# Kernel tuning notes

Hardware: AMD Instinct MI355X
Metric: run time of the kernel (lower is better)

## Reference

```python
import jax, jax.numpy as jnp
import numpy as np

K = 8            # hard-attention top-k neighbors per node
NEG_SLOPE = 0.2  # leaky relu slope


def setup_inputs() -> dict:
    key = jax.random.key(0)
    k1, k2, k3, k4, k5, k6 = jax.random.split(key, 6)
    N, D, F = 50000, 64, 256
    H, O = 8, 32
    feat = jax.random.normal(k1, (N, F), dtype=jnp.float32)
    neighbors = jax.random.randint(k2, (N, D), 0, N)  # src node ids per dst
    # learned params (xavier-normal-ish scale)
    p = jax.random.normal(k3, (1, F), dtype=jnp.float32) * float(np.sqrt(2.0 / (1 + F)))
    W = jax.random.normal(k4, (F, H * O), dtype=jnp.float32) * float(np.sqrt(2.0 / (F + H * O)))
    attn_l = jax.random.normal(k5, (1, H, O), dtype=jnp.float32) * float(np.sqrt(2.0 / (H * O + 1)))
    attn_r = jax.random.normal(k6, (1, H, O), dtype=jnp.float32) * float(np.sqrt(2.0 / (H * O + 1)))
    return {"feat": feat, "neighbors": neighbors, "p": p, "W": W,
            "attn_l": attn_l, "attn_r": attn_r}


def reference(feat, neighbors, p, W, attn_l, attn_r):
    N, F = feat.shape
    H, O = attn_l.shape[1], attn_l.shape[2]
    # node projection score y = |p . x| / ||p||
    y = jnp.abs(feat @ p[0]) / jnp.linalg.norm(p)          # [N]
    # hard top-k neighbor selection by source score (select_topk on 'y')
    ys = y[neighbors]                                       # [N, D]
    _, idx = jax.lax.top_k(ys, K)                           # [N, K]
    src = jnp.take_along_axis(neighbors, idx, axis=1)       # [N, K] source ids
    # gating + projection
    gate = jax.nn.sigmoid(y) * 2.0                          # [N]
    ft = ((gate[:, None] * feat) @ W).reshape(N, H, O)      # [N, H, O]
    el = jnp.sum(ft * attn_l, axis=-1)                      # [N, H]
    er = jnp.sum(ft * attn_r, axis=-1)                      # [N, H]
    # edge scores: u_add_v, leaky_relu, edge_softmax over each dst's K edges
    e = el[src] + er[:, None, :]                            # [N, K, H]
    e = jnp.where(e > 0, e, NEG_SLOPE * e)
    a = jax.nn.softmax(e, axis=1)                           # [N, K, H]
    # u_mul_e + sum aggregation
    rst = jnp.einsum('nkh,nkho->nho', a, ft[src])           # [N, H, O]
    return jax.nn.elu(rst)
```

## Files before the change

kernel.cpp:

```cpp
#include <hip/hip_runtime.h>
#include <math.h>

#define NEG_SLOPE 0.2f

typedef _Float16 half8 __attribute__((ext_vector_type(8)));
typedef float floatx4 __attribute__((ext_vector_type(4)));

__device__ __forceinline__ float dot4f(float4 a, float4 b) {
    return a.x * b.x + a.y * b.y + a.z * b.z + a.w * b.w;
}

static __device__ __forceinline__ unsigned short f2h(float x) {
    _Float16 h = (_Float16)x;
    return __builtin_bit_cast(unsigned short, h);
}
static __device__ __forceinline__ float h2f(unsigned short u) {
    _Float16 h = __builtin_bit_cast(_Float16, u);
    return (float)h;
}

__global__ void k_prepw(const float* __restrict__ W, unsigned short* __restrict__ Wtp) {
    const int c = blockIdx.x;
    const int k = threadIdx.x;
    float v = W[(size_t)k * 256 + c];
    Wtp[(size_t)(c >> 4) * 4096 + (k >> 3) * 128 + (c & 15) * 8 + (k & 7)] = f2h(v);
}

__global__ __launch_bounds__(256) void k_fused(const float4* __restrict__ feat4,
                                               const float4* __restrict__ p4,
                                               const unsigned short* __restrict__ Wtp,
                                               float* __restrict__ y,
                                               unsigned short* __restrict__ fth,
                                               int N) {
    __shared__ unsigned short As[16][264];
    const int lane = threadIdx.x & 63;
    const int w = threadIdx.x >> 6;
    const int l16 = lane & 15, quad = lane >> 4;
    const int nb = blockIdx.x * 16;

    const float4 p = p4[lane];
    float pp = dot4f(p, p);
#pragma unroll
    for (int off = 32; off; off >>= 1) pp += __shfl_xor(pp, off, 64);
    const float rnorm = 1.0f / sqrtf(pp);

#pragma unroll
    for (int j = 0; j < 4; ++j) {
        const int m = w * 4 + j;
        int n = nb + m;
        const bool valid = n < N;
        if (!valid) n = N - 1;
        float4 f = feat4[(size_t)n * 64 + lane];
        float dp = dot4f(f, p);
#pragma unroll
        for (int off = 32; off; off >>= 1) dp += __shfl_xor(dp, off, 64);
        float yv = fabsf(dp) * rnorm;
        if (lane == 0 && valid) y[n] = yv;
        float g = 2.0f / (1.0f + expf(-yv));
        ushort4 u;
        u.x = f2h(g * f.x);
        u.y = f2h(g * f.y);
        u.z = f2h(g * f.z);
        u.w = f2h(g * f.w);
        *(ushort4*)&As[m][lane * 4] = u;
    }
    __syncthreads();

    floatx4 acc[4];
#pragma unroll
    for (int ct = 0; ct < 4; ++ct) acc[ct] = (floatx4){0.f, 0.f, 0.f, 0.f};

    const unsigned short* bbase = Wtp + (size_t)(w * 4) * 4096 + quad * 128 + l16 * 8;

    for (int ks = 0; ks < 256; ks += 32) {
        half8 a = *(const half8*)&As[l16][ks + quad * 8];
        const unsigned short* bk = bbase + (ks >> 3) * 128;
        half8 b0 = *(const half8*)(bk);
        half8 b1 = *(const half8*)(bk + 4096);
        half8 b2 = *(const half8*)(bk + 8192);
        half8 b3 = *(const half8*)(bk + 12288);
        acc[0] = __builtin_amdgcn_mfma_f32_16x16x32_f16(a, b0, acc[0], 0, 0, 0);
        acc[1] = __builtin_amdgcn_mfma_f32_16x16x32_f16(a, b1, acc[1], 0, 0, 0);
        acc[2] = __builtin_amdgcn_mfma_f32_16x16x32_f16(a, b2, acc[2], 0, 0, 0);
        acc[3] = __builtin_amdgcn_mfma_f32_16x16x32_f16(a, b3, acc[3], 0, 0, 0);
    }

#pragma unroll
    for (int ct = 0; ct < 4; ++ct)
#pragma unroll
        for (int i = 0; i < 4; ++i) {
            int row = nb + quad * 4 + i;
            if (row < N)
                fth[(size_t)row * 256 + w * 64 + ct * 16 + l16] = f2h(acc[ct][i]);
        }
}

__global__ __launch_bounds__(256) void k_aggr(const int* __restrict__ nbr,
                                              const float* __restrict__ y,
                                              const uint2* __restrict__ fth2,
                                              const float4* __restrict__ al4,
                                              const float4* __restrict__ ar4,
                                              float4* __restrict__ out4,
                                              int N) {
    const int lane = threadIdx.x & 63;
    const int n = blockIdx.x * 4 + (threadIdx.x >> 6);
    if (n >= N) return;

    const int s = nbr[(size_t)n * 64 + lane];
    const unsigned int key = __float_as_uint(y[s]);

    unsigned int t = 0u;
#pragma unroll
    for (int b = 31; b >= 0; --b) {
        unsigned int cand = t | (1u << b);
        unsigned long long m = __ballot(key >= cand);
        if (__popcll(m) >= 8) t = cand;
    }
    const unsigned long long gtmask = __ballot(key > t);
    const int ngt = __popcll(gtmask);
    const unsigned long long eqmask = __ballot(key == t);
    const unsigned long long below = (1ull << lane) - 1ull;
    const int eqrank = __popcll(eqmask & below);
    const bool in8 = (key > t) | ((key == t) & (eqrank < 8 - ngt));
    unsigned long long selmask = __ballot(in8);

    int srck[8];
#pragma unroll
    for (int k = 0; k < 8; ++k) {
        int l = __ffsll((long long)selmask) - 1;
        srck[k] = __shfl(s, l, 64);
        selmask &= selmask - 1ull;
    }

    float4 ftn, ftk[8];
    {
        uint2 v = fth2[(size_t)n * 64 + lane];
        ftn.x = h2f((unsigned short)(v.x & 0xffff));
        ftn.y = h2f((unsigned short)(v.x >> 16));
        ftn.z = h2f((unsigned short)(v.y & 0xffff));
        ftn.w = h2f((unsigned short)(v.y >> 16));
    }
#pragma unroll
    for (int k = 0; k < 8; ++k) {
        uint2 v = fth2[(size_t)srck[k] * 64 + lane];
        ftk[k].x = h2f((unsigned short)(v.x & 0xffff));
        ftk[k].y = h2f((unsigned short)(v.x >> 16));
        ftk[k].z = h2f((unsigned short)(v.y & 0xffff));
        ftk[k].w = h2f((unsigned short)(v.y >> 16));
    }

    const float4 al = al4[lane];
    const float4 ar = ar4[lane];

    float er = dot4f(ftn, ar);
#pragma unroll
    for (int off = 1; off < 8; off <<= 1) er += __shfl_xor(er, off, 64);

    float e[8];
#pragma unroll
    for (int k = 0; k < 8; ++k) {
        float el = dot4f(ftk[k], al);
#pragma unroll
        for (int off = 1; off < 8; off <<= 1) el += __shfl_xor(el, off, 64);
        float ev = el + er;
        e[k] = ev > 0.f ? ev : NEG_SLOPE * ev;
    }

    float m = e[0];
#pragma unroll
    for (int k = 1; k < 8; ++k) m = fmaxf(m, e[k]);
    float sum = 0.f;
#pragma unroll
    for (int k = 0; k < 8; ++k) {
        e[k] = expf(e[k] - m);
        sum += e[k];
    }
    const float inv = 1.0f / sum;

    float4 acc = make_float4(0.f, 0.f, 0.f, 0.f);
#pragma unroll
    for (int k = 0; k < 8; ++k) {
        float a = e[k] * inv;
        acc.x += a * ftk[k].x;
        acc.y += a * ftk[k].y;
        acc.z += a * ftk[k].z;
        acc.w += a * ftk[k].w;
    }
    acc.x = acc.x > 0.f ? acc.x : expf(acc.x) - 1.f;
    acc.y = acc.y > 0.f ? acc.y : expf(acc.y) - 1.f;
    acc.z = acc.z > 0.f ? acc.z : expf(acc.z) - 1.f;
    acc.w = acc.w > 0.f ? acc.w : expf(acc.w) - 1.f;
    out4[(size_t)n * 64 + lane] = acc;
}

extern "C" void kernel_launch(void* const* d_in, const int* in_sizes, int n_in,
                              void* d_out, int out_size, void* d_ws, size_t ws_size,
                              hipStream_t stream) {
    const float* feat = (const float*)d_in[0];
    const int* nbr    = (const int*)d_in[1];
    const float* p    = (const float*)d_in[2];
    const float* W    = (const float*)d_in[3];
    const float* al   = (const float*)d_in[4];
    const float* ar   = (const float*)d_in[5];
    float* out = (float*)d_out;

    const int N = in_sizes[0] / 256;

    float* y = (float*)d_ws;
    unsigned short* Wtp = (unsigned short*)(y + N);
    unsigned short* fth = Wtp + 256 * 256;

    k_prepw<<<256, 256, 0, stream>>>(W, Wtp);
    k_fused<<<(N + 15) / 16, 256, 0, stream>>>((const float4*)feat, (const float4*)p,
                                               Wtp, y, fth, N);
    k_aggr<<<(N + 3) / 4, 256, 0, stream>>>(nbr, y, (const uint2*)fth,
                                            (const float4*)al, (const float4*)ar,
                                            (float4*)out, N);
}
```

Before: 176.6 us.

## Precompute el/er in GEMM epilogue, double GEMM row tile, use fast exp

The projection kernel now handles 32 rows per block (two MFMA M-tiles reusing each loaded W fragment). It stages the fp16 result in shared memory and computes the per-head attention terms el and er there, writing them to workspace. The aggregation kernel then reads el/er instead of recomputing dot products and shuffle reductions for each of the 8 neighbors, and it no longer loads the destination row's features. Other changes: __expf replaces expf, and the top-k bit search skips the sign bit. These add workspace traffic and shared-memory use and slightly reduce exp accuracy.

```diff
diff --git a/kernel.cpp b/kernel.cpp
--- a/kernel.cpp
+++ b/kernel.cpp
@@ -29,14 +29,18 @@
 __global__ __launch_bounds__(256) void k_fused(const float4* __restrict__ feat4,
                                                const float4* __restrict__ p4,
                                                const unsigned short* __restrict__ Wtp,
+                                               const float4* __restrict__ al4,
+                                               const float4* __restrict__ ar4,
                                                float* __restrict__ y,
                                                unsigned short* __restrict__ fth,
+                                               float* __restrict__ el,
+                                               float* __restrict__ er,
                                                int N) {
-    __shared__ unsigned short As[16][264];
+    __shared__ unsigned short As[32][264];
     const int lane = threadIdx.x & 63;
     const int w = threadIdx.x >> 6;
     const int l16 = lane & 15, quad = lane >> 4;
-    const int nb = blockIdx.x * 16;
+    const int nb = blockIdx.x * 32;
 
     const float4 p = p4[lane];
     float pp = dot4f(p, p);
@@ -45,8 +49,8 @@
     const float rnorm = 1.0f / sqrtf(pp);
 
 #pragma unroll
-    for (int j = 0; j < 4; ++j) {
-        const int m = w * 4 + j;
+    for (int j = 0; j < 8; ++j) {
+        const int m = w * 8 + j;
         int n = nb + m;
         const bool valid = n < N;
         if (!valid) n = N - 1;
@@ -56,7 +60,7 @@
         for (int off = 32; off; off >>= 1) dp += __shfl_xor(dp, off, 64);
         float yv = fabsf(dp) * rnorm;
         if (lane == 0 && valid) y[n] = yv;
-        float g = 2.0f / (1.0f + expf(-yv));
+        float g = 2.0f / (1.0f + __expf(-yv));
         ushort4 u;
         u.x = f2h(g * f.x);
         u.y = f2h(g * f.y);
@@ -66,52 +70,83 @@
     }
     __syncthreads();
 
-    floatx4 acc[4];
-#pragma unroll
-    for (int ct = 0; ct < 4; ++ct) acc[ct] = (floatx4){0.f, 0.f, 0.f, 0.f};
+    floatx4 acc[2][4];
+#pragma unroll
+    for (int mt = 0; mt < 2; ++mt)
+#pragma unroll
+        for (int ct = 0; ct < 4; ++ct) acc[mt][ct] = (floatx4){0.f, 0.f, 0.f, 0.f};
 
     const unsigned short* bbase = Wtp + (size_t)(w * 4) * 4096 + quad * 128 + l16 * 8;
 
     for (int ks = 0; ks < 256; ks += 32) {
-        half8 a = *(const half8*)&As[l16][ks + quad * 8];
+        half8 a0 = *(const half8*)&As[l16][ks + quad * 8];
+        half8 a1 = *(const half8*)&As[16 + l16][ks + quad * 8];
         const unsigned short* bk = bbase + (ks >> 3) * 128;
         half8 b0 = *(const half8*)(bk);
         half8 b1 = *(const half8*)(bk + 4096);
         half8 b2 = *(const half8*)(bk + 8192);
         half8 b3 = *(const half8*)(bk + 12288);
-        acc[0] = __builtin_amdgcn_mfma_f32_16x16x32_f16(a, b0, acc[0], 0, 0, 0);
-        acc[1] = __builtin_amdgcn_mfma_f32_16x16x32_f16(a, b1, acc[1], 0, 0, 0);
-        acc[2] = __builtin_amdgcn_mfma_f32_16x16x32_f16(a, b2, acc[2], 0, 0, 0);
-        acc[3] = __builtin_amdgcn_mfma_f32_16x16x32_f16(a, b3, acc[3], 0, 0, 0);
-    }
-
-#pragma unroll
-    for (int ct = 0; ct < 4; ++ct)
-#pragma unroll
-        for (int i = 0; i < 4; ++i) {
-            int row = nb + quad * 4 + i;
-            if (row < N)
-                fth[(size_t)row * 256 + w * 64 + ct * 16 + l16] = f2h(acc[ct][i]);
+        acc[0][0] = __builtin_amdgcn_mfma_f32_16x16x32_f16(a0, b0, acc[0][0], 0, 0, 0);
+        acc[0][1] = __builtin_amdgcn_mfma_f32_16x16x32_f16(a0, b1, acc[0][1], 0, 0, 0);
+        acc[0][2] = __builtin_amdgcn_mfma_f32_16x16x32_f16(a0, b2, acc[0][2], 0, 0, 0);
+        acc[0][3] = __builtin_amdgcn_mfma_f32_16x16x32_f16(a0, b3, acc[0][3], 0, 0, 0);
+        acc[1][0] = __builtin_amdgcn_mfma_f32_16x16x32_f16(a1, b0, acc[1][0], 0, 0, 0);
+        acc[1][1] = __builtin_amdgcn_mfma_f32_16x16x32_f16(a1, b1, acc[1][1], 0, 0, 0);
+        acc[1][2] = __builtin_amdgcn_mfma_f32_16x16x32_f16(a1, b2, acc[1][2], 0, 0, 0);
+        acc[1][3] = __builtin_amdgcn_mfma_f32_16x16x32_f16(a1, b3, acc[1][3], 0, 0, 0);
+    }
+
+    __syncthreads();
+#pragma unroll
+    for (int mt = 0; mt < 2; ++mt)
+#pragma unroll
+        for (int ct = 0; ct < 4; ++ct)
+#pragma unroll
+            for (int i = 0; i < 4; ++i) {
+                int row = mt * 16 + quad * 4 + i;
+                int col = w * 64 + ct * 16 + l16;
+                unsigned short h = f2h(acc[mt][ct][i]);
+                As[row][col] = h;
+                int grow = nb + row;
+                if (grow < N) fth[(size_t)grow * 256 + col] = h;
+            }
+    __syncthreads();
+
+#pragma unroll
+    for (int t2 = 0; t2 < 2; ++t2) {
+        const int m = threadIdx.x & 31;
+        const int h = (threadIdx.x >> 5) & 7;
+        const float4* att = t2 ? ar4 : al4;
+        float d = 0.f;
+#pragma unroll
+        for (int o4 = 0; o4 < 8; ++o4) {
+            ushort4 u = *(const ushort4*)&As[m][h * 32 + o4 * 4];
+            float4 a = att[h * 8 + o4];
+            d += h2f(u.x) * a.x + h2f(u.y) * a.y + h2f(u.z) * a.z + h2f(u.w) * a.w;
         }
+        int n = nb + m;
+        if (n < N) (t2 ? er : el)[(size_t)n * 8 + h] = d;
+    }
 }
 
 __global__ __launch_bounds__(256) void k_aggr(const int* __restrict__ nbr,
                                               const float* __restrict__ y,
                                               const uint2* __restrict__ fth2,
-                                              const float4* __restrict__ al4,
-                                              const float4* __restrict__ ar4,
+                                              const float* __restrict__ el,
+                                              const float* __restrict__ er,
                                               float4* __restrict__ out4,
                                               int N) {
     const int lane = threadIdx.x & 63;
     const int n = blockIdx.x * 4 + (threadIdx.x >> 6);
     if (n >= N) return;
+    const int h = lane >> 3;
 
     const int s = nbr[(size_t)n * 64 + lane];
     const unsigned int key = __float_as_uint(y[s]);
 
     unsigned int t = 0u;
 #pragma unroll
-    for (int b = 31; b >= 0; --b) {
+    for (int b = 30; b >= 0; --b) {
         unsigned int cand = t | (1u << b);
         unsigned long long m = __ballot(key >= cand);
         if (__popcll(m) >= 8) t = cand;
@@ -132,14 +167,7 @@
         selmask &= selmask - 1ull;
     }
 
-    float4 ftn, ftk[8];
-    {
-        uint2 v = fth2[(size_t)n * 64 + lane];
-        ftn.x = h2f((unsigned short)(v.x & 0xffff));
-        ftn.y = h2f((unsigned short)(v.x >> 16));
-        ftn.z = h2f((unsigned short)(v.y & 0xffff));
-        ftn.w = h2f((unsigned short)(v.y >> 16));
-    }
+    float4 ftk[8];
 #pragma unroll
     for (int k = 0; k < 8; ++k) {
         uint2 v = fth2[(size_t)srck[k] * 64 + lane];
@@ -148,21 +176,11 @@
         ftk[k].z = h2f((unsigned short)(v.y & 0xffff));
         ftk[k].w = h2f((unsigned short)(v.y >> 16));
     }
-
-    const float4 al = al4[lane];
-    const float4 ar = ar4[lane];
-
-    float er = dot4f(ftn, ar);
-#pragma unroll
-    for (int off = 1; off < 8; off <<= 1) er += __shfl_xor(er, off, 64);
-
+    const float erv = er[(size_t)n * 8 + h];
     float e[8];
 #pragma unroll
     for (int k = 0; k < 8; ++k) {
-        float el = dot4f(ftk[k], al);
-#pragma unroll
-        for (int off = 1; off < 8; off <<= 1) el += __shfl_xor(el, off, 64);
-        float ev = el + er;
+        float ev = el[(size_t)srck[k] * 8 + h] + erv;
         e[k] = ev > 0.f ? ev : NEG_SLOPE * ev;
     }
 
@@ -172,7 +190,7 @@
     float sum = 0.f;
 #pragma unroll
     for (int k = 0; k < 8; ++k) {
-        e[k] = expf(e[k] - m);
+        e[k] = __expf(e[k] - m);
         sum += e[k];
     }
     const float inv = 1.0f / sum;
@@ -186,10 +204,10 @@
         acc.z += a * ftk[k].z;
         acc.w += a * ftk[k].w;
     }
-    acc.x = acc.x > 0.f ? acc.x : expf(acc.x) - 1.f;
-    acc.y = acc.y > 0.f ? acc.y : expf(acc.y) - 1.f;
-    acc.z = acc.z > 0.f ? acc.z : expf(acc.z) - 1.f;
-    acc.w = acc.w > 0.f ? acc.w : expf(acc.w) - 1.f;
+    acc.x = acc.x > 0.f ? acc.x : __expf(acc.x) - 1.f;
+    acc.y = acc.y > 0.f ? acc.y : __expf(acc.y) - 1.f;
+    acc.z = acc.z > 0.f ? acc.z : __expf(acc.z) - 1.f;
+    acc.w = acc.w > 0.f ? acc.w : __expf(acc.w) - 1.f;
     out4[(size_t)n * 64 + lane] = acc;
 }
 
@@ -208,12 +226,14 @@
 
     float* y = (float*)d_ws;
     unsigned short* Wtp = (unsigned short*)(y + N);
-    unsigned short* fth = Wtp + 256 * 256;
+    float* el = (float*)(Wtp + 256 * 256);
+    float* er = el + (size_t)N * 8;
+    unsigned short* fth = (unsigned short*)(er + (size_t)N * 8);
 
     k_prepw<<<256, 256, 0, stream>>>(W, Wtp);
-    k_fused<<<(N + 15) / 16, 256, 0, stream>>>((const float4*)feat, (const float4*)p,
-                                               Wtp, y, fth, N);
-    k_aggr<<<(N + 3) / 4, 256, 0, stream>>>(nbr, y, (const uint2*)fth,
-                                            (const float4*)al, (const float4*)ar,
+    k_fused<<<(N + 31) / 32, 256, 0, stream>>>((const float4*)feat, (const float4*)p,
+                                               Wtp, (const float4*)al, (const float4*)ar,
+                                               y, fth, el, er, N);
+    k_aggr<<<(N + 3) / 4, 256, 0, stream>>>(nbr, y, (const uint2*)fth, el, er,
                                             (float4*)out, N);
 }
```

Result: no change. 177.8 us (+0.7%).
